# Kernel optimization log

Hardware: AMD Instinct MI355X
Metric: run time of the kernel (lower is better)

Reference implementation:

```python
import jax, jax.numpy as jnp
import numpy as np
import math

D_MODEL = 1024
N_HEADS = 16
HEAD_DIM = D_MODEL // N_HEADS


def get_slopes(n_heads: int) -> jnp.ndarray:
    def pow2_slopes(n):
        start = 2.0 ** (-8.0 / n)
        return np.array([start * start ** i for i in range(n)], dtype=np.float32)
    if math.log2(n_heads).is_integer():
        return jnp.asarray(pow2_slopes(n_heads))
    closest = 2 ** math.floor(math.log2(n_heads))
    base = pow2_slopes(closest)
    extra = pow2_slopes(2 * closest)[::2][: n_heads - closest]
    return jnp.asarray(np.concatenate([base, extra]))


def setup_inputs() -> dict:
    key = jax.random.key(0)
    ks = jax.random.split(key, 9)
    s = 1.0 / math.sqrt(D_MODEL)
    x = jax.random.normal(ks[0], (2, 2048, D_MODEL), dtype=jnp.float32)
    q_w = jax.random.uniform(ks[1], (D_MODEL, D_MODEL), jnp.float32, -s, s)
    q_b = jax.random.uniform(ks[2], (D_MODEL,), jnp.float32, -s, s)
    k_w = jax.random.uniform(ks[3], (D_MODEL, D_MODEL), jnp.float32, -s, s)
    k_b = jax.random.uniform(ks[4], (D_MODEL,), jnp.float32, -s, s)
    v_w = jax.random.uniform(ks[5], (D_MODEL, D_MODEL), jnp.float32, -s, s)
    v_b = jax.random.uniform(ks[6], (D_MODEL,), jnp.float32, -s, s)
    o_w = jax.random.uniform(ks[7], (D_MODEL, D_MODEL), jnp.float32, -s, s)
    o_b = jax.random.uniform(ks[8], (D_MODEL,), jnp.float32, -s, s)
    return {"x": x, "q_w": q_w, "q_b": q_b, "k_w": k_w, "k_b": k_b,
            "v_w": v_w, "v_b": v_b, "o_w": o_w, "o_b": o_b}


def reference(x, q_w, q_b, k_w, k_b, v_w, v_b, o_w, o_b):
    B, S, D = x.shape
    H, hd = N_HEADS, HEAD_DIM
    # torch Linear: y = x @ W.T + b
    Q = (x @ q_w.T + q_b).reshape(B, S, H, hd).transpose(0, 2, 1, 3)  # [B,H,S,hd]
    K = (x @ k_w.T + k_b).reshape(B, S, H, hd).transpose(0, 2, 1, 3)
    V = (x @ v_w.T + v_b).reshape(B, S, H, hd).transpose(0, 2, 1, 3)
    scores = jnp.einsum('bhqd,bhkd->bhqk', Q, K) / math.sqrt(hd)
    # ALiBi bias: slopes[h] * (k_pos - q_pos)
    pos = jnp.arange(S)
    rel = (pos[None, :] - pos[:, None]).astype(scores.dtype)  # [S,S]
    slopes = get_slopes(H)
    scores = scores + slopes[None, :, None, None] * rel[None, None, :, :]
    # causal mask
    causal = pos[None, :] <= pos[:, None]  # [S,S] True where allowed
    scores = jnp.where(causal[None, None], scores, -jnp.inf)
    attn = jax.nn.softmax(scores, axis=-1)  # dropout=0 (eval)
    out = jnp.einsum('bhqk,bhkd->bhqd', attn, V)
    out = out.transpose(0, 2, 1, 3).reshape(B, S, D)
    return out @ o_w.T + o_b
```

## Files before the change

kernel.cpp:

```cpp
#include <hip/hip_runtime.h>
#include <hip/hip_bf16.h>

typedef __attribute__((ext_vector_type(8))) short short8;
typedef __attribute__((ext_vector_type(4))) float float4v;
typedef __attribute__((ext_vector_type(4))) short short4v;
typedef __attribute__((ext_vector_type(4))) unsigned int uint4v;
typedef __attribute__((ext_vector_type(2))) unsigned int uint2v;

#define B_ 2
#define S_ 2048
#define D_ 1024
#define H_ 16
#define HD_ 64
#define M_ 4096
#define LOG2E 1.442695040888963f

__device__ __forceinline__ unsigned short f2bf(float f) {
  unsigned int u = __builtin_bit_cast(unsigned int, f);
  u += 0x7fffu + ((u >> 16) & 1u);
  return (unsigned short)(u >> 16);
}

__device__ __forceinline__ unsigned int pkbf(float a, float b) {
  __hip_bfloat162 h = __float22bfloat162_rn(make_float2(a, b));
  unsigned int u;
  __builtin_memcpy(&u, &h, sizeof(u));
  return u;
}

__device__ __forceinline__ float max3f(float a, float b, float c) {
  return fmaxf(fmaxf(a, b), c);
}

__device__ __forceinline__ void gload_lds16(const void* g, void* l) {
  __builtin_amdgcn_global_load_lds(
      (const __attribute__((address_space(1))) void*)g,
      (__attribute__((address_space(3))) void*)l, 16, 0, 0);
}

__global__ __launch_bounds__(256, 4) void cvt_kernel(
    const float* __restrict__ x,  const float* __restrict__ qw,
    const float* __restrict__ kw, const float* __restrict__ vw,
    const float* __restrict__ ow, unsigned short* __restrict__ dst)
{
  const int seg = blockIdx.y;
  const float* src;
  size_t doff;
  if (seg < 4)       { src = x + (size_t)seg * 1048576; doff = (size_t)seg * 1048576; }
  else if (seg == 4) { src = qw; doff = 4194304u; }
  else if (seg == 5) { src = kw; doff = 4194304u + 1048576u; }
  else if (seg == 6) { src = vw; doff = 4194304u + 2097152u; }
  else               { src = ow; doff = 4194304u + 3145728u; }
  const size_t i = ((size_t)blockIdx.x * 256 + threadIdx.x) * 4;
  float4v v = *(const float4v*)(src + i);
  short4v p;
#pragma unroll
  for (int r = 0; r < 4; ++r) p[r] = (short)f2bf(v[r]);
  *(short4v*)(dst + doff + i) = p;
}

template <int TN>
__global__ __launch_bounds__(256, 3) void gemm_kernel(
    const unsigned short* __restrict__ X,
    const unsigned short* __restrict__ W0, const unsigned short* __restrict__ W1,
    const unsigned short* __restrict__ W2,
    const float* __restrict__ Bi0, const float* __restrict__ Bi1,
    const float* __restrict__ Bi2,
    unsigned short* O0, unsigned short* O1, unsigned short* O2,
    float* OutF, int md0, int md1, int md2)
{
  constexpr int NJ = TN / 32;
  constexpr int SMEM = (TN == 128) ? (32 * 132 * 4) : (8192 + TN * 64);
  const int z = blockIdx.z;
  const unsigned short* W  = (z == 0) ? W0  : ((z == 1) ? W1  : W2);
  const float* Bi          = (z == 0) ? Bi0 : ((z == 1) ? Bi1 : Bi2);
  unsigned short* Out      = (z == 0) ? O0  : ((z == 1) ? O1  : O2);
  const int mode           = (z == 0) ? md0 : ((z == 1) ? md1 : md2);

  __shared__ __align__(16) char smem[SMEM];
  char* As = smem;
  char* Bs = smem + 8192;
  float* tb = (float*)smem;

  const int t = threadIdx.x, l = t & 63;
  const int w = t >> 6, lr = l & 15, lg = l >> 4;
  const int n0 = blockIdx.x * TN, m0 = blockIdx.y * 128;
  const int wm = (w >> 1) * 64, wn = (w & 1) * (TN / 2);

  float4v acc[4][NJ];
#pragma unroll
  for (int i = 0; i < 4; ++i)
#pragma unroll
    for (int j = 0; j < NJ; ++j) acc[i][j] = (float4v){0.f, 0.f, 0.f, 0.f};

  const int c0 = t, c1 = t + 256;
  const int r0 = c0 >> 2, k80 = (c0 & 3) * 8;
  const int r1 = c1 >> 2, k81 = (c1 & 3) * 8;

  for (int k0 = 0; k0 < 1024; k0 += 32) {
    __syncthreads();
    gload_lds16(X + (size_t)(m0 + r0) * 1024 + k0 + k80, As + c0 * 16);
    gload_lds16(X + (size_t)(m0 + r1) * 1024 + k0 + k81, As + c1 * 16);
    gload_lds16(W + (size_t)(n0 + r0) * 1024 + k0 + k80, Bs + c0 * 16);
    if (TN == 128)
      gload_lds16(W + (size_t)(n0 + r1) * 1024 + k0 + k81, Bs + c1 * 16);
    __syncthreads();

    short8 af[4], bfr[NJ];
#pragma unroll
    for (int i = 0; i < 4; ++i)
      af[i] = *(const short8*)(As + (wm + i * 16 + lr) * 64 + lg * 16);
#pragma unroll
    for (int j = 0; j < NJ; ++j)
      bfr[j] = *(const short8*)(Bs + (wn + j * 16 + lr) * 64 + lg * 16);
#pragma unroll
    for (int i = 0; i < 4; ++i)
#pragma unroll
      for (int j = 0; j < NJ; ++j)
        acc[i][j] = __builtin_amdgcn_mfma_f32_16x16x32_bf16(af[i], bfr[j], acc[i][j], 0, 0, 0);
  }

  float bv[NJ];
#pragma unroll
  for (int j = 0; j < NJ; ++j) bv[j] = Bi[n0 + wn + j * 16 + lr];

  if constexpr (TN == 128) {
    if (mode == 1) {
      __syncthreads();
      const int rbase = (w >> 1) * 16;
      const int row16 = t >> 3, chunk = t & 7;
#pragma unroll
      for (int i = 0; i < 4; ++i) {
#pragma unroll
        for (int j = 0; j < 4; ++j)
#pragma unroll
          for (int r = 0; r < 4; ++r)
            tb[(rbase + lg * 4 + r) * 132 + wn + j * 16 + lr] = acc[i][j][r] + bv[j];
        __syncthreads();
        const int grow = m0 + ((row16 < 16) ? (i * 16 + row16) : (64 + i * 16 + row16 - 16));
        const int b = grow >> 11, sl = grow & 2047;
        const int colg = n0 + chunk * 16;
        const int hh = colg >> 6, d0 = colg & 63;
        float4v v4[4];
#pragma unroll
        for (int q = 0; q < 4; ++q)
          v4[q] = *(const float4v*)(tb + row16 * 132 + chunk * 16 + q * 4);
        uint4v lo, hi;
#pragma unroll
        for (int q = 0; q < 2; ++q) {
          lo[q * 2]     = pkbf(v4[q][0], v4[q][1]);
          lo[q * 2 + 1] = pkbf(v4[q][2], v4[q][3]);
          hi[q * 2]     = pkbf(v4[q + 2][0], v4[q + 2][1]);
          hi[q * 2 + 1] = pkbf(v4[q + 2][2], v4[q + 2][3]);
        }
        unsigned short* dst = Out + ((size_t)(b * H_ + hh) * S_ + sl) * HD_ + d0;
        *(short8*)dst = __builtin_bit_cast(short8, lo);
        *(short8*)(dst + 8) = __builtin_bit_cast(short8, hi);
        __syncthreads();
      }
      return;
    }
    if (mode == 2) {
#pragma unroll
      for (int i = 0; i < 4; ++i) {
        const int rowb = m0 + wm + i * 16 + lg * 4;
#pragma unroll
        for (int j = 0; j < 4; ++j) {
          const int col = n0 + wn + j * 16 + lr;
          const int b = rowb >> 11, s = rowb & 2047;
          const int hh = col >> 6, d = col & 63;
          const int gI = (s >> 2) & 7;
          const int gP = ((gI & 3) << 1) | (gI >> 2);
          const int sN = (s & ~31) | (gP << 2);
          uint2v pk2;
          pk2[0] = pkbf(acc[i][j][0] + bv[j], acc[i][j][1] + bv[j]);
          pk2[1] = pkbf(acc[i][j][2] + bv[j], acc[i][j][3] + bv[j]);
          *(short4v*)(Out + ((size_t)(b * H_ + hh) * HD_ + d) * S_ + sN) =
              __builtin_bit_cast(short4v, pk2);
        }
      }
      return;
    }
  }
#pragma unroll
  for (int i = 0; i < 4; ++i) {
    const int rowb = m0 + wm + i * 16 + lg * 4;
#pragma unroll
    for (int j = 0; j < NJ; ++j) {
      const int col = n0 + wn + j * 16 + lr;
#pragma unroll
      for (int r = 0; r < 4; ++r)
        OutF[(size_t)(rowb + r) * 1024 + col] = acc[i][j][r] + bv[j];
    }
  }
}

__global__ __launch_bounds__(256, 4) void attn_kernel(
    const unsigned short* __restrict__ Q, const unsigned short* __restrict__ K,
    const unsigned short* __restrict__ VT, unsigned short* __restrict__ O)
{
  __shared__ __align__(16) char smem[32768];

  const int t = threadIdx.x, l = t & 63;
  const int w = t >> 6, lr = l & 15, lg = l >> 4;
  const int bh = blockIdx.x;
  const int it = 31 - (int)blockIdx.y;
  const int h = bh & 15;

  const unsigned short* qbp = Q + (size_t)bh * S_ * HD_;
  const unsigned short* kbp = K + (size_t)bh * S_ * HD_;
  const unsigned short* vbp = VT + (size_t)bh * HD_ * S_;

  const float slope2 = __builtin_amdgcn_exp2f(-0.5f * (float)(h + 1)) * LOG2E;
  const float qksc = 0.125f * LOG2E;

  const int g0 = t, g1 = t + 256;
  const int sr0 = g0 >> 3, sc0 = (g0 & 7) ^ (sr0 & 7);
  const int sr1 = g1 >> 3, sc1 = (g1 & 7) ^ (sr1 & 7);

  const int fchunk = ((4 + lg) ^ (lr & 7)) * 16;
  const int fchunk0 = ((lg) ^ (lr & 7)) * 16;

  const int qrow = it * 64 + w * 16;
  const int qpos = qrow + lr;

  short8 ones;
#pragma unroll
  for (int e = 0; e < 8; ++e) ones[e] = (short)0x3F80;

  short8 qf[2];
#pragma unroll
  for (int ks = 0; ks < 2; ++ks)
    qf[ks] = *(const short8*)(qbp + (size_t)(qrow + lr) * HD_ + ks * 32 + lg * 8);

  float kb[16];
#pragma unroll
  for (int nj = 0; nj < 4; ++nj)
#pragma unroll
    for (int r = 0; r < 4; ++r)
      kb[nj * 4 + r] = slope2 * (float)(nj * 16 + lg * 4 + r);
  float jb = 0.0f;
  const float jbstep = slope2 * 64.0f;

  const float4v z4 = (float4v){0.f, 0.f, 0.f, 0.f};

  float4v o_acc[4], l_acc;
#pragma unroll
  for (int dt = 0; dt < 4; ++dt) o_acc[dt] = z4;
  l_acc = z4;
  float m_st = -1e30f;

  gload_lds16(kbp + (size_t)sr0 * HD_ + sc0 * 8, smem + g0 * 16);
  gload_lds16(kbp + (size_t)sr1 * HD_ + sc1 * 8, smem + g1 * 16);
  gload_lds16(vbp + (size_t)sr0 * S_ + sc0 * 8, smem + 16384 + g0 * 16);
  gload_lds16(vbp + (size_t)sr1 * S_ + sc1 * 8, smem + 16384 + g1 * 16);
  __syncthreads();

  const int vcl = lr & 7;

  for (int j = 0; j <= it; ++j) {
    const int cur = j & 1;
    char* Ks = smem + (cur ? 8192 : 0);
    char* Vs = smem + 16384 + (cur ? 8192 : 0);
    if (j < it) {
      char* Kn = smem + (cur ? 0 : 8192);
      char* Vn = smem + 16384 + (cur ? 0 : 8192);
      const int jn = j + 1;
      gload_lds16(kbp + (size_t)(jn * 64 + sr0) * HD_ + sc0 * 8, Kn + g0 * 16);
      gload_lds16(kbp + (size_t)(jn * 64 + sr1) * HD_ + sc1 * 8, Kn + g1 * 16);
      gload_lds16(vbp + (size_t)sr0 * S_ + jn * 64 + sc0 * 8, Vn + g0 * 16);
      gload_lds16(vbp + (size_t)sr1 * S_ + jn * 64 + sc1 * 8, Vn + g1 * 16);
    }

    float4v s_acc[4];
#pragma unroll
    for (int nj = 0; nj < 4; ++nj) {
      short8 kf0 = *(const short8*)(Ks + (nj * 16 + lr) * 128 + fchunk0);
      float4v t0 = __builtin_amdgcn_mfma_f32_16x16x32_bf16(kf0, qf[0], z4, 0, 0, 0);
      short8 kf1 = *(const short8*)(Ks + (nj * 16 + lr) * 128 + fchunk);
      s_acc[nj] = __builtin_amdgcn_mfma_f32_16x16x32_bf16(kf1, qf[1], t0, 0, 0, 0);
    }

#pragma unroll
    for (int nj = 0; nj < 4; ++nj)
#pragma unroll
      for (int r = 0; r < 4; ++r)
        s_acc[nj][r] = s_acc[nj][r] * qksc + kb[nj * 4 + r];
    if (j == it) {
#pragma unroll
      for (int nj = 0; nj < 4; ++nj)
#pragma unroll
        for (int r = 0; r < 4; ++r) {
          const int kpos = j * 64 + nj * 16 + lg * 4 + r;
          if (kpos > qpos) s_acc[nj][r] = -1e30f;
        }
    }

    float a0 = max3f(s_acc[0][0], s_acc[0][1], s_acc[0][2]);
    float a1 = max3f(s_acc[0][3], s_acc[1][0], s_acc[1][1]);
    float a2 = max3f(s_acc[1][2], s_acc[1][3], s_acc[2][0]);
    float a3 = max3f(s_acc[2][1], s_acc[2][2], s_acc[2][3]);
    float a4 = max3f(s_acc[3][0], s_acc[3][1], s_acc[3][2]);
    float b0 = max3f(a0, a1, a2);
    float b1 = max3f(a3, a4, s_acc[3][3]);
    float mxt = fmaxf(b0, b1);
    mxt = fmaxf(mxt, __shfl_xor(mxt, 16, 64));
    mxt = fmaxf(mxt, __shfl_xor(mxt, 32, 64));
    const float mx = mxt + jb;
    if (__any(mx > m_st + 8.0f)) {
      const float mn = fmaxf(m_st, mx);
      const float alpha = __builtin_amdgcn_exp2f(m_st - mn);
      m_st = mn;
#pragma unroll
      for (int dt = 0; dt < 4; ++dt)
#pragma unroll
        for (int r = 0; r < 4; ++r) o_acc[dt][r] *= alpha;
#pragma unroll
      for (int r = 0; r < 4; ++r) l_acc[r] *= alpha;
    }
    const float c1 = m_st - jb;
#pragma unroll
    for (int nj = 0; nj < 4; ++nj)
#pragma unroll
      for (int r = 0; r < 4; ++r)
        s_acc[nj][r] = __builtin_amdgcn_exp2f(s_acc[nj][r] - c1);

    short8 pT[2];
#pragma unroll
    for (int njp = 0; njp < 2; ++njp) {
      uint4v u;
      u[0] = pkbf(s_acc[njp * 2][0], s_acc[njp * 2][1]);
      u[1] = pkbf(s_acc[njp * 2][2], s_acc[njp * 2][3]);
      u[2] = pkbf(s_acc[njp * 2 + 1][0], s_acc[njp * 2 + 1][1]);
      u[3] = pkbf(s_acc[njp * 2 + 1][2], s_acc[njp * 2 + 1][3]);
      pT[njp] = __builtin_bit_cast(short8, u);
    }

    l_acc = __builtin_amdgcn_mfma_f32_16x16x32_bf16(ones, pT[0], l_acc, 0, 0, 0);
    l_acc = __builtin_amdgcn_mfma_f32_16x16x32_bf16(ones, pT[1], l_acc, 0, 0, 0);

#pragma unroll
    for (int dt = 0; dt < 4; ++dt) {
      const char* rowp = Vs + (dt * 16 + lr) * 128;
#pragma unroll
      for (int njp = 0; njp < 2; ++njp) {
        short8 vf8 = *(const short8*)(rowp + (((njp * 4 + lg) ^ vcl) << 4));
        o_acc[dt] = __builtin_amdgcn_mfma_f32_16x16x32_bf16(vf8, pT[njp], o_acc[dt], 0, 0, 0);
      }
    }
    jb += jbstep;
    __syncthreads();
  }

  char* tw = smem + w * 4416;
#pragma unroll
  for (int dt = 0; dt < 4; ++dt)
#pragma unroll
    for (int r = 0; r < 4; ++r)
      *(float*)(tw + ((dt * 16 + lg * 4 + r) * 17 + lr) * 4) = o_acc[dt][r];
  if (lg == 0) *(float*)(tw + 4352 + lr * 4) = l_acc[0];

  const int q2 = l >> 2, dbase = (l & 3) * 16;
  const float invl = 1.0f / *(const float*)(tw + 4352 + q2 * 4);
  uint4v os0, os1;
#pragma unroll
  for (int k = 0; k < 8; ++k) {
    const float va = *(const float*)(tw + ((dbase + 2 * k) * 17 + q2) * 4) * invl;
    const float vb = *(const float*)(tw + ((dbase + 2 * k + 1) * 17 + q2) * 4) * invl;
    if (k < 4) os0[k] = pkbf(va, vb); else os1[k - 4] = pkbf(va, vb);
  }
  const int brow = (bh >> 4) * S_;
  unsigned short* op = O + (size_t)(brow + qrow + q2) * 1024 + h * 64 + dbase;
  *(short8*)op = __builtin_bit_cast(short8, os0);
  *(short8*)(op + 8) = __builtin_bit_cast(short8, os1);
}

extern "C" void kernel_launch(void* const* d_in, const int* in_sizes, int n_in,
                              void* d_out, int out_size, void* d_ws, size_t ws_size,
                              hipStream_t stream) {
  (void)in_sizes; (void)n_in; (void)out_size; (void)ws_size;
  const float* x  = (const float*)d_in[0];
  const float* qw = (const float*)d_in[1];
  const float* qb = (const float*)d_in[2];
  const float* kw = (const float*)d_in[3];
  const float* kb = (const float*)d_in[4];
  const float* vw = (const float*)d_in[5];
  const float* vb = (const float*)d_in[6];
  const float* ow = (const float*)d_in[7];
  const float* ob = (const float*)d_in[8];
  float* out = (float*)d_out;

  unsigned short* xb  = (unsigned short*)d_ws;
  unsigned short* qwb = xb  + (size_t)M_ * D_;
  unsigned short* kwb = qwb + (size_t)D_ * D_;
  unsigned short* vwb = kwb + (size_t)D_ * D_;
  unsigned short* owb = vwb + (size_t)D_ * D_;
  unsigned short* qws = owb + (size_t)D_ * D_;
  unsigned short* kws = qws + (size_t)M_ * D_;
  unsigned short* vws = kws + (size_t)M_ * D_;
  unsigned short* aws = vws + (size_t)M_ * D_;

  cvt_kernel<<<dim3(1024, 8), dim3(256), 0, stream>>>(x, qw, kw, vw, ow, xb);
  gemm_kernel<128><<<dim3(8, 32, 3), dim3(256), 0, stream>>>(
      xb, qwb, kwb, vwb, qb, kb, vb, qws, kws, vws, out, 1, 1, 2);
  attn_kernel<<<dim3(32, 32), dim3(256), 0, stream>>>(qws, kws, vws, aws);
  gemm_kernel<64><<<dim3(16, 32, 1), dim3(256), 0, stream>>>(
      aws, owb, owb, owb, ob, ob, ob, aws, aws, aws, out, 0, 0, 0);
}
```

Before: 179.8 us.

## Process two query tiles per attention block and swizzle GEMM block order

Each attention workgroup now handles two adjacent 64-row query tiles (128 rows), so every K/V tile loaded into LDS feeds twice as many MFMAs. This halves the grid and lowers the occupancy hint to 2. MFMA sections are wrapped with s_setprio to favour matrix issue. The GEMM kernels also remap block indices with an XCD-aware swizzle to improve L2 locality. The cost is higher register pressure, fewer blocks for load balance, and some extra epilogue LDS traffic.

```diff
diff --git a/kernel.cpp b/kernel.cpp
--- a/kernel.cpp
+++ b/kernel.cpp
@@ -71,6 +71,8 @@
 {
   constexpr int NJ = TN / 32;
   constexpr int SMEM = (TN == 128) ? (32 * 132 * 4) : (8192 + TN * 64);
+  constexpr int GX = (TN == 128) ? 8 : 16;
+  constexpr int CPX = (GX * 32) / 8;
   const int z = blockIdx.z;
   const unsigned short* W  = (z == 0) ? W0  : ((z == 1) ? W1  : W2);
   const float* Bi          = (z == 0) ? Bi0 : ((z == 1) ? Bi1 : Bi2);
@@ -84,7 +86,10 @@
 
   const int t = threadIdx.x, l = t & 63;
   const int w = t >> 6, lr = l & 15, lg = l >> 4;
-  const int n0 = blockIdx.x * TN, m0 = blockIdx.y * 128;
+
+  const int bid = (int)blockIdx.y * GX + (int)blockIdx.x;
+  const int sw  = (bid & 7) * CPX + (bid >> 3);
+  const int n0 = (sw % GX) * TN, m0 = (sw / GX) * 128;
   const int wm = (w >> 1) * 64, wn = (w & 1) * (TN / 2);
 
   float4v acc[4][NJ];
@@ -195,7 +200,7 @@
   }
 }
 
-__global__ __launch_bounds__(256, 4) void attn_kernel(
+__global__ __launch_bounds__(256, 2) void attn_kernel(
     const unsigned short* __restrict__ Q, const unsigned short* __restrict__ K,
     const unsigned short* __restrict__ VT, unsigned short* __restrict__ O)
 {
@@ -204,8 +209,9 @@
   const int t = threadIdx.x, l = t & 63;
   const int w = t >> 6, lr = l & 15, lg = l >> 4;
   const int bh = blockIdx.x;
-  const int it = 31 - (int)blockIdx.y;
+  const int it = 15 - (int)blockIdx.y;
   const int h = bh & 15;
+  const int jmax = 2 * it + 1;
 
   const unsigned short* qbp = Q + (size_t)bh * S_ * HD_;
   const unsigned short* kbp = K + (size_t)bh * S_ * HD_;
@@ -221,17 +227,21 @@
   const int fchunk = ((4 + lg) ^ (lr & 7)) * 16;
   const int fchunk0 = ((lg) ^ (lr & 7)) * 16;
 
-  const int qrow = it * 64 + w * 16;
-  const int qpos = qrow + lr;
+  const int qrowA = it * 128 + w * 16;
+  const int qrowB = qrowA + 64;
+  const int qposA = qrowA + lr;
+  const int qposB = qrowB + lr;
 
   short8 ones;
 #pragma unroll
   for (int e = 0; e < 8; ++e) ones[e] = (short)0x3F80;
 
-  short8 qf[2];
-#pragma unroll
-  for (int ks = 0; ks < 2; ++ks)
-    qf[ks] = *(const short8*)(qbp + (size_t)(qrow + lr) * HD_ + ks * 32 + lg * 8);
+  short8 qfA[2], qfB[2];
+#pragma unroll
+  for (int ks = 0; ks < 2; ++ks) {
+    qfA[ks] = *(const short8*)(qbp + (size_t)(qrowA + lr) * HD_ + ks * 32 + lg * 8);
+    qfB[ks] = *(const short8*)(qbp + (size_t)(qrowB + lr) * HD_ + ks * 32 + lg * 8);
+  }
 
   float kb[16];
 #pragma unroll
@@ -244,11 +254,68 @@
 
   const float4v z4 = (float4v){0.f, 0.f, 0.f, 0.f};
 
-  float4v o_acc[4], l_acc;
-#pragma unroll
-  for (int dt = 0; dt < 4; ++dt) o_acc[dt] = z4;
-  l_acc = z4;
-  float m_st = -1e30f;
+  float4v oA[4], oB[4], lA, lB;
+#pragma unroll
+  for (int dt = 0; dt < 4; ++dt) { oA[dt] = z4; oB[dt] = z4; }
+  lA = z4; lB = z4;
+  float mA = -1e30f, mB = -1e30f;
+
+  int j = 0;
+
+  auto sm = [&](float4v (&s)[4], float& mst, float4v& lac, float4v (&oac)[4],
+                bool domask, int qpos, short8 (&pT)[2]) {
+#pragma unroll
+    for (int nj = 0; nj < 4; ++nj)
+#pragma unroll
+      for (int r = 0; r < 4; ++r)
+        s[nj][r] = s[nj][r] * qksc + kb[nj * 4 + r];
+    if (domask) {
+#pragma unroll
+      for (int nj = 0; nj < 4; ++nj)
+#pragma unroll
+        for (int r = 0; r < 4; ++r) {
+          const int kpos = j * 64 + nj * 16 + lg * 4 + r;
+          if (kpos > qpos) s[nj][r] = -1e30f;
+        }
+    }
+    float a0 = max3f(s[0][0], s[0][1], s[0][2]);
+    float a1 = max3f(s[0][3], s[1][0], s[1][1]);
+    float a2 = max3f(s[1][2], s[1][3], s[2][0]);
+    float a3 = max3f(s[2][1], s[2][2], s[2][3]);
+    float a4 = max3f(s[3][0], s[3][1], s[3][2]);
+    float b0 = max3f(a0, a1, a2);
+    float b1 = max3f(a3, a4, s[3][3]);
+    float mxt = fmaxf(b0, b1);
+    mxt = fmaxf(mxt, __shfl_xor(mxt, 16, 64));
+    mxt = fmaxf(mxt, __shfl_xor(mxt, 32, 64));
+    const float mx = mxt + jb;
+    if (__any(mx > mst + 8.0f)) {
+      const float mn = fmaxf(mst, mx);
+      const float alpha = __builtin_amdgcn_exp2f(mst - mn);
+      mst = mn;
+#pragma unroll
+      for (int dt = 0; dt < 4; ++dt)
+#pragma unroll
+        for (int r = 0; r < 4; ++r) oac[dt][r] *= alpha;
+#pragma unroll
+      for (int r = 0; r < 4; ++r) lac[r] *= alpha;
+    }
+    const float c1 = mst - jb;
+#pragma unroll
+    for (int nj = 0; nj < 4; ++nj)
+#pragma unroll
+      for (int r = 0; r < 4; ++r)
+        s[nj][r] = __builtin_amdgcn_exp2f(s[nj][r] - c1);
+#pragma unroll
+    for (int njp = 0; njp < 2; ++njp) {
+      uint4v u;
+      u[0] = pkbf(s[njp * 2][0], s[njp * 2][1]);
+      u[1] = pkbf(s[njp * 2][2], s[njp * 2][3]);
+      u[2] = pkbf(s[njp * 2 + 1][0], s[njp * 2 + 1][1]);
+      u[3] = pkbf(s[njp * 2 + 1][2], s[njp * 2 + 1][3]);
+      pT[njp] = __builtin_bit_cast(short8, u);
+    }
+  };
 
   gload_lds16(kbp + (size_t)sr0 * HD_ + sc0 * 8, smem + g0 * 16);
   gload_lds16(kbp + (size_t)sr1 * HD_ + sc1 * 8, smem + g1 * 16);
@@ -258,11 +325,11 @@
 
   const int vcl = lr & 7;
 
-  for (int j = 0; j <= it; ++j) {
+  for (j = 0; j <= jmax; ++j) {
     const int cur = j & 1;
     char* Ks = smem + (cur ? 8192 : 0);
     char* Vs = smem + 16384 + (cur ? 8192 : 0);
-    if (j < it) {
+    if (j < jmax) {
       char* Kn = smem + (cur ? 0 : 8192);
       char* Vn = smem + 16384 + (cur ? 0 : 8192);
       const int jn = j + 1;
@@ -271,73 +338,34 @@
       gload_lds16(vbp + (size_t)sr0 * S_ + jn * 64 + sc0 * 8, Vn + g0 * 16);
       gload_lds16(vbp + (size_t)sr1 * S_ + jn * 64 + sc1 * 8, Vn + g1 * 16);
     }
-
-    float4v s_acc[4];
+    const bool aOn = (j < jmax);
+
+    float4v sA[4], sB[4];
+    __builtin_amdgcn_s_setprio(1);
 #pragma unroll
     for (int nj = 0; nj < 4; ++nj) {
       short8 kf0 = *(const short8*)(Ks + (nj * 16 + lr) * 128 + fchunk0);
-      float4v t0 = __builtin_amdgcn_mfma_f32_16x16x32_bf16(kf0, qf[0], z4, 0, 0, 0);
       short8 kf1 = *(const short8*)(Ks + (nj * 16 + lr) * 128 + fchunk);
-      s_acc[nj] = __builtin_amdgcn_mfma_f32_16x16x32_bf16(kf1, qf[1], t0, 0, 0, 0);
-    }
-
-#pragma unroll
-    for (int nj = 0; nj < 4; ++nj)
-#pragma unroll
-      for (int r = 0; r < 4; ++r)
-        s_acc[nj][r] = s_acc[nj][r] * qksc + kb[nj * 4 + r];
-    if (j == it) {
-#pragma unroll
-      for (int nj = 0; nj < 4; ++nj)
-#pragma unroll
-        for (int r = 0; r < 4; ++r) {
-          const int kpos = j * 64 + nj * 16 + lg * 4 + r;
-          if (kpos > qpos) s_acc[nj][r] = -1e30f;
-        }
-    }
-
-    float a0 = max3f(s_acc[0][0], s_acc[0][1], s_acc[0][2]);
-    float a1 = max3f(s_acc[0][3], s_acc[1][0], s_acc[1][1]);
-    float a2 = max3f(s_acc[1][2], s_acc[1][3], s_acc[2][0]);
-    float a3 = max3f(s_acc[2][1], s_acc[2][2], s_acc[2][3]);
-    float a4 = max3f(s_acc[3][0], s_acc[3][1], s_acc[3][2]);
-    float b0 = max3f(a0, a1, a2);
-    float b1 = max3f(a3, a4, s_acc[3][3]);
-    float mxt = fmaxf(b0, b1);
-    mxt = fmaxf(mxt, __shfl_xor(mxt, 16, 64));
-    mxt = fmaxf(mxt, __shfl_xor(mxt, 32, 64));
-    const float mx = mxt + jb;
-    if (__any(mx > m_st + 8.0f)) {
-      const float mn = fmaxf(m_st, mx);
-      const float alpha = __builtin_amdgcn_exp2f(m_st - mn);
-      m_st = mn;
-#pragma unroll
-      for (int dt = 0; dt < 4; ++dt)
-#pragma unroll
-        for (int r = 0; r < 4; ++r) o_acc[dt][r] *= alpha;
-#pragma unroll
-      for (int r = 0; r < 4; ++r) l_acc[r] *= alpha;
-    }
-    const float c1 = m_st - jb;
-#pragma unroll
-    for (int nj = 0; nj < 4; ++nj)
-#pragma unroll
-      for (int r = 0; r < 4; ++r)
-        s_acc[nj][r] = __builtin_amdgcn_exp2f(s_acc[nj][r] - c1);
-
-    short8 pT[2];
-#pragma unroll
-    for (int njp = 0; njp < 2; ++njp) {
-      uint4v u;
-      u[0] = pkbf(s_acc[njp * 2][0], s_acc[njp * 2][1]);
-      u[1] = pkbf(s_acc[njp * 2][2], s_acc[njp * 2][3]);
-      u[2] = pkbf(s_acc[njp * 2 + 1][0], s_acc[njp * 2 + 1][1]);
-      u[3] = pkbf(s_acc[njp * 2 + 1][2], s_acc[njp * 2 + 1][3]);
-      pT[njp] = __builtin_bit_cast(short8, u);
-    }
-
-    l_acc = __builtin_amdgcn_mfma_f32_16x16x32_bf16(ones, pT[0], l_acc, 0, 0, 0);
-    l_acc = __builtin_amdgcn_mfma_f32_16x16x32_bf16(ones, pT[1], l_acc, 0, 0, 0);
+      if (aOn) {
+        float4v ta = __builtin_amdgcn_mfma_f32_16x16x32_bf16(kf0, qfA[0], z4, 0, 0, 0);
+        sA[nj] = __builtin_amdgcn_mfma_f32_16x16x32_bf16(kf1, qfA[1], ta, 0, 0, 0);
+      }
+      float4v tb2 = __builtin_amdgcn_mfma_f32_16x16x32_bf16(kf0, qfB[0], z4, 0, 0, 0);
+      sB[nj] = __builtin_amdgcn_mfma_f32_16x16x32_bf16(kf1, qfB[1], tb2, 0, 0, 0);
+    }
+    __builtin_amdgcn_s_setprio(0);
+
+    short8 pTA[2], pTB[2];
+    if (aOn) sm(sA, mA, lA, oA, j == jmax - 1, qposA, pTA);
+    sm(sB, mB, lB, oB, j == jmax, qposB, pTB);
+
+    __builtin_amdgcn_s_setprio(1);
+    if (aOn) {
+      lA = __builtin_amdgcn_mfma_f32_16x16x32_bf16(ones, pTA[0], lA, 0, 0, 0);
+      lA = __builtin_amdgcn_mfma_f32_16x16x32_bf16(ones, pTA[1], lA, 0, 0, 0);
+    }
+    lB = __builtin_amdgcn_mfma_f32_16x16x32_bf16(ones, pTB[0], lB, 0, 0, 0);
+    lB = __builtin_amdgcn_mfma_f32_16x16x32_bf16(ones, pTB[1], lB, 0, 0, 0);
 
 #pragma unroll
     for (int dt = 0; dt < 4; ++dt) {
@@ -345,34 +373,41 @@
 #pragma unroll
       for (int njp = 0; njp < 2; ++njp) {
         short8 vf8 = *(const short8*)(rowp + (((njp * 4 + lg) ^ vcl) << 4));
-        o_acc[dt] = __builtin_amdgcn_mfma_f32_16x16x32_bf16(vf8, pT[njp], o_acc[dt], 0, 0, 0);
+        if (aOn)
+          oA[dt] = __builtin_amdgcn_mfma_f32_16x16x32_bf16(vf8, pTA[njp], oA[dt], 0, 0, 0);
+        oB[dt] = __builtin_amdgcn_mfma_f32_16x16x32_bf16(vf8, pTB[njp], oB[dt], 0, 0, 0);
       }
     }
+    __builtin_amdgcn_s_setprio(0);
     jb += jbstep;
     __syncthreads();
   }
 
-  char* tw = smem + w * 4416;
-#pragma unroll
-  for (int dt = 0; dt < 4; ++dt)
-#pragma unroll
-    for (int r = 0; r < 4; ++r)
-      *(float*)(tw + ((dt * 16 + lg * 4 + r) * 17 + lr) * 4) = o_acc[dt][r];
-  if (lg == 0) *(float*)(tw + 4352 + lr * 4) = l_acc[0];
-
-  const int q2 = l >> 2, dbase = (l & 3) * 16;
-  const float invl = 1.0f / *(const float*)(tw + 4352 + q2 * 4);
-  uint4v os0, os1;
-#pragma unroll
-  for (int k = 0; k < 8; ++k) {
-    const float va = *(const float*)(tw + ((dbase + 2 * k) * 17 + q2) * 4) * invl;
-    const float vb = *(const float*)(tw + ((dbase + 2 * k + 1) * 17 + q2) * 4) * invl;
-    if (k < 4) os0[k] = pkbf(va, vb); else os1[k - 4] = pkbf(va, vb);
-  }
   const int brow = (bh >> 4) * S_;
-  unsigned short* op = O + (size_t)(brow + qrow + q2) * 1024 + h * 64 + dbase;
-  *(short8*)op = __builtin_bit_cast(short8, os0);
-  *(short8*)(op + 8) = __builtin_bit_cast(short8, os1);
+  auto epi = [&](float4v (&oac)[4], float4v& lac, int qrow) {
+    char* tw = smem + w * 4416;
+#pragma unroll
+    for (int dt = 0; dt < 4; ++dt)
+#pragma unroll
+      for (int r = 0; r < 4; ++r)
+        *(float*)(tw + ((dt * 16 + lg * 4 + r) * 17 + lr) * 4) = oac[dt][r];
+    if (lg == 0) *(float*)(tw + 4352 + lr * 4) = lac[0];
+
+    const int q2 = l >> 2, dbase = (l & 3) * 16;
+    const float invl = 1.0f / *(const float*)(tw + 4352 + q2 * 4);
+    uint4v os0, os1;
+#pragma unroll
+    for (int k = 0; k < 8; ++k) {
+      const float va = *(const float*)(tw + ((dbase + 2 * k) * 17 + q2) * 4) * invl;
+      const float vb = *(const float*)(tw + ((dbase + 2 * k + 1) * 17 + q2) * 4) * invl;
+      if (k < 4) os0[k] = pkbf(va, vb); else os1[k - 4] = pkbf(va, vb);
+    }
+    unsigned short* op = O + (size_t)(brow + qrow + q2) * 1024 + h * 64 + dbase;
+    *(short8*)op = __builtin_bit_cast(short8, os0);
+    *(short8*)(op + 8) = __builtin_bit_cast(short8, os1);
+  };
+  epi(oA, lA, qrowA);
+  epi(oB, lB, qrowB);
 }
 
 extern "C" void kernel_launch(void* const* d_in, const int* in_sizes, int n_in,
@@ -403,7 +438,7 @@
   cvt_kernel<<<dim3(1024, 8), dim3(256), 0, stream>>>(x, qw, kw, vw, ow, xb);
   gemm_kernel<128><<<dim3(8, 32, 3), dim3(256), 0, stream>>>(
       xb, qwb, kwb, vwb, qb, kb, vb, qws, kws, vws, out, 1, 1, 2);
-  attn_kernel<<<dim3(32, 32), dim3(256), 0, stream>>>(qws, kws, vws, aws);
+  attn_kernel<<<dim3(32, 16), dim3(256), 0, stream>>>(qws, kws, vws, aws);
   gemm_kernel<64><<<dim3(16, 32, 1), dim3(256), 0, stream>>>(
       aws, owb, owb, owb, ob, ob, ob, aws, aws, aws, out, 0, 0, 0);
 }
```

Result: slower. 199.2 us (+10.8%).
